# Kernel optimization log

Measured on AMD Instinct MI355X. Metric: run time of the kernel, lower is better.

The kernel has to match this reference:

```python
import jax, jax.numpy as jnp
import numpy as np

FM = 128       # feature_maps
QM = 128       # query_maps
ROUNDS = 4     # test_rounds (training=False)
N_VARS = 24576
N_CLAUSES = 98304
N_EDGES = 3 * N_CLAUSES
EPS = 1e-6


def _dense(k, fan_in, fan_out):
    return jax.random.normal(k, (fan_in, fan_out), jnp.float32) * (1.0 / np.sqrt(fan_in))


def setup_inputs() -> dict:
    key = jax.random.key(0)
    ks = jax.random.split(key, 20)
    return {
        "edge_lit": jax.random.randint(ks[0], (N_EDGES,), 0, 2 * N_VARS, dtype=jnp.int32),
        "edge_clause": jnp.sort(jax.random.randint(ks[1], (N_EDGES,), 0, N_CLAUSES, dtype=jnp.int32)),
        "noise_v": jax.random.normal(ks[2], (ROUNDS, N_VARS, 4), jnp.float32),
        "noise_c": jax.random.normal(ks[3], (ROUNDS, N_CLAUSES, 4), jnp.float32),
        # variables_query: MLP(2, QM, QM), input FM+4
        "vq_w0": _dense(ks[4], FM + 4, QM), "vq_b0": jnp.zeros((QM,), jnp.float32),
        "vq_w1": _dense(ks[5], QM, QM),     "vq_b1": jnp.zeros((QM,), jnp.float32),
        # clauses_query: MLP(2, QM, QM), input FM+4
        "cq_w0": _dense(ks[6], FM + 4, QM), "cq_b0": jnp.zeros((QM,), jnp.float32),
        "cq_w1": _dense(ks[7], QM, QM),     "cq_b1": jnp.zeros((QM,), jnp.float32),
        # clause_update: MLP(2, 2*FM, FM+QM), input FM+2*QM=384
        "cm_w0": _dense(ks[8], FM + 2 * QM, 2 * FM), "cm_b0": jnp.zeros((2 * FM,), jnp.float32),
        "cm_w1": _dense(ks[9], 2 * FM, FM + QM),     "cm_b1": jnp.zeros((FM + QM,), jnp.float32),
        # update_gate: MLP(3, 2*FM, FM), input QM+FM+2*QM=512
        "ug_w0": _dense(ks[10], QM + FM + 2 * QM, 2 * FM), "ug_b0": jnp.zeros((2 * FM,), jnp.float32),
        "ug_w1": _dense(ks[11], 2 * FM, 2 * FM),           "ug_b1": jnp.zeros((2 * FM,), jnp.float32),
        "ug_w2": _dense(ks[12], 2 * FM, FM),               "ug_b2": jnp.zeros((FM,), jnp.float32),
        # clauses_mask_output: MLP(2, FM, 1)
        "co_w0": _dense(ks[13], FM, FM), "co_b0": jnp.zeros((FM,), jnp.float32),
        "co_w1": _dense(ks[14], FM, 1),  "co_b1": jnp.zeros((1,), jnp.float32),
        "n_vars": N_VARS,
        "n_clauses": N_CLAUSES,
    }


def _forward(edge_lit, edge_clause, n_vars, n_clauses, floats):
    (noise_v, noise_c,
     vq_w0, vq_b0, vq_w1, vq_b1,
     cq_w0, cq_b0, cq_w1, cq_b1,
     cm_w0, cm_b0, cm_w1, cm_b1,
     ug_w0, ug_b0, ug_w1, ug_b1, ug_w2, ug_b2,
     co_w0, co_b0, co_w1, co_b1) = floats

    n_edges = edge_lit.shape[0]
    # lit_degree = row sums of sparse adjacency (all nonzeros are 1.0)
    lit_degree = jax.ops.segment_sum(jnp.ones((n_edges,), jnp.float32), edge_lit,
                                     num_segments=2 * n_vars)[:, None]          # [2V,1]
    degree_weight = jax.lax.rsqrt(jnp.maximum(lit_degree, 1.0))
    var_degree_weight = 4.0 * jax.lax.rsqrt(
        jnp.maximum(lit_degree[:n_vars] + lit_degree[n_vars:], 1.0))            # [V,1]

    def mlp2(x, w0, b0, w1, b1):
        return jax.nn.relu(x @ w0 + b0) @ w1 + b1

    def mlp3(x, w0, b0, w1, b1, w2, b2):
        h = jax.nn.relu(x @ w0 + b0)
        h = jax.nn.relu(h @ w1 + b1)
        return h @ w2 + b2

    def pair_norm(x):
        # PairNorm(subtract_mean=True), single graph -> global mean over nodes
        x = x - jnp.mean(x, axis=0, keepdims=True)
        return x * jax.lax.rsqrt(jnp.mean(jnp.square(x)) + EPS)

    def clauses_loss_fn(vq, cq):
        # unsat_cnf_clauses_loss: softplus literal values aggregated per clause,
        # clause satisfiability exp(-sum), gated by clause query mask.
        lits = jax.nn.softplus(jnp.concatenate([vq, -vq], axis=0))              # [2V,Q]
        csum = jax.ops.segment_sum(lits[edge_lit], edge_clause,
                                   num_segments=n_clauses)                      # [C,Q]
        loss = jnp.exp(-csum) * jax.nn.sigmoid(cq)
        return jnp.mean(loss), loss

    grad_fn = jax.grad(clauses_loss_fn, argnums=(0, 1), has_aux=True)

    def step(carry, xs):
        variables, clauses = carry
        nv, nc = xs
        vq = mlp2(jnp.concatenate([variables, nv], -1), vq_w0, vq_b0, vq_w1, vq_b1)
        cq = mlp2(jnp.concatenate([clauses, nc], -1), cq_w0, cq_b0, cq_w1, cq_b1)
        (vgrad, cgrad), clauses_loss = grad_fn(vq, cq)
        vgrad = vgrad * var_degree_weight
        clauses_loss = clauses_loss * 4.0
        clause_data = mlp2(jnp.concatenate([clauses, clauses_loss, cgrad], -1),
                           cm_w0, cm_b0, cm_w1, cm_b1)                          # [C,FM+QM]
        variables_loss_all = clause_data[:, :QM]
        clauses = pair_norm(clause_data[:, QM:]) * 0.25 + 0.1 * clauses
        # adj_matrix @ variables_loss_all (literal-side aggregation)
        variables_loss = jax.ops.segment_sum(variables_loss_all[edge_clause], edge_lit,
                                             num_segments=2 * n_vars) * degree_weight
        unit = jnp.concatenate([vgrad, variables,
                                variables_loss[:n_vars], variables_loss[n_vars:]], -1)
        variables = pair_norm(mlp3(unit, ug_w0, ug_b0, ug_w1, ug_b1, ug_w2, ug_b2)) * 0.25 \
                    + 0.1 * variables
        logits = mlp2(clauses, co_w0, co_b0, co_w1, co_b1)[:, 0]                # [C]
        return (variables, clauses), logits

    init = (jnp.ones((n_vars, FM), jnp.float32), jnp.ones((n_clauses, FM), jnp.float32))
    _, logits = jax.lax.scan(step, init, (noise_v, noise_c))                    # [R,C]
    return jax.nn.sigmoid(logits), jax.nn.softplus(logits)


def reference(edge_lit, edge_clause, noise_v, noise_c,
              vq_w0, vq_b0, vq_w1, vq_b1,
              cq_w0, cq_b0, cq_w1, cq_b1,
              cm_w0, cm_b0, cm_w1, cm_b1,
              ug_w0, ug_b0, ug_w1, ug_b1, ug_w2, ug_b2,
              co_w0, co_b0, co_w1, co_b1,
              n_vars, n_clauses):
    floats = (noise_v, noise_c,
              vq_w0, vq_b0, vq_w1, vq_b1,
              cq_w0, cq_b0, cq_w1, cq_b1,
              cm_w0, cm_b0, cm_w1, cm_b1,
              ug_w0, ug_b0, ug_w1, ug_b1, ug_w2, ug_b2,
              co_w0, co_b0, co_w1, co_b1)
    return _forward(edge_lit, edge_clause, int(n_vars), int(n_clauses), floats)
```

## Files before the change

### kernel.cpp

```cpp
#include <hip/hip_runtime.h>
#include <math.h>

#define NV 24576
#define NC 98304
#define NE 294912
#define CMCHUNK 24576

typedef unsigned short bf16;
typedef _Float16 f16;
using bf8 = __attribute__((ext_vector_type(8))) short;
using f4  = __attribute__((ext_vector_type(4))) float;

static constexpr float INV_CQM = 1.0f / 12582912.0f;
static constexpr float LOG2E = 1.44269504f;
static constexpr float LN2 = 0.69314718f;

__device__ __forceinline__ float b2f(bf16 h) { return __uint_as_float(((unsigned)h) << 16); }
__device__ __forceinline__ bf16 f2b(float f) {
  unsigned u = __float_as_uint(f);
  u += 0x7fff + ((u >> 16) & 1);
  return (bf16)(u >> 16);
}
__device__ __forceinline__ float fexp2(float x) { float r; asm("v_exp_f32 %0, %1" : "=v"(r) : "v"(x)); return r; }
__device__ __forceinline__ float flog2(float x) { float r; asm("v_log_f32 %0, %1" : "=v"(r) : "v"(x)); return r; }
__device__ __forceinline__ float frcpf(float x) { float r; asm("v_rcp_f32 %0, %1" : "=v"(r) : "v"(x)); return r; }
__device__ __forceinline__ float fsigm(float x) { return frcpf(1.0f + fexp2(-x * LOG2E)); }
__device__ __forceinline__ float fsoftplus(float x) {
  return fmaxf(x, 0.0f) + LN2 * flog2(1.0f + fexp2(-fabsf(x) * LOG2E));
}
__device__ __forceinline__ float cvt_ld(float x) { return x; }
__device__ __forceinline__ float cvt_ld(bf16 x) { return b2f(x); }

__device__ __forceinline__ void gload16(const void* g, void* l) {
  __builtin_amdgcn_global_load_lds((const __attribute__((address_space(1))) unsigned int*)g,
                                   (__attribute__((address_space(3))) unsigned int*)l, 16, 0, 0);
}


__global__ __launch_bounds__(256) void k_cptr(const int* __restrict__ ec, int* __restrict__ ptr) {
  int c = blockIdx.x * 256 + threadIdx.x;
  if (c > NC) return;
  int lo = 0, hi = NE;
  while (lo < hi) { int mid = (lo + hi) >> 1; if (ec[mid] < c) lo = mid + 1; else hi = mid; }
  ptr[c] = lo;
}

__global__ __launch_bounds__(256) void k_litcnt(const int* __restrict__ el, int* __restrict__ cnt) {
  int e = blockIdx.x * 256 + threadIdx.x;
  atomicAdd(&cnt[el[e]], 1);
}

__global__ __launch_bounds__(1024) void k_scan(int* __restrict__ cnt, int* __restrict__ ptr) {
  __shared__ int wsum[16];
  __shared__ int carry_s;
  int tid = threadIdx.x, lane = tid & 63, w = tid >> 6;
  if (tid == 0) carry_s = 0;
  __syncthreads();
  for (int base = 0; base < 2 * NV; base += 1024) {
    int x = cnt[base + tid];
    int v = x;
#pragma unroll
    for (int off = 1; off < 64; off <<= 1) {
      int y = __shfl_up(v, off, 64);
      if (lane >= off) v += y;
    }
    if (lane == 63) wsum[w] = v;
    __syncthreads();
    int carry = carry_s;
    int wpre = 0;
    for (int i = 0; i < w; ++i) wpre += wsum[i];
    int excl = carry + wpre + (v - x);
    ptr[base + tid] = excl;
    cnt[base + tid] = excl;
    __syncthreads();
    if (tid == 1023) carry_s = carry + wpre + v;
  }
  __syncthreads();
  if (tid == 0) ptr[2 * NV] = carry_s;
}

__global__ __launch_bounds__(256) void k_fillsort(const int* __restrict__ el, const int* __restrict__ ec,
                                                  int* __restrict__ cur, int* __restrict__ lclause) {
  int e = blockIdx.x * 256 + threadIdx.x;
  int pos = atomicAdd(&cur[el[e]], 1);
  lclause[pos] = ec[e];
}

__global__ __launch_bounds__(256) void k_degree(const int* __restrict__ lptr, float* __restrict__ dw,
                                                float* __restrict__ vdw) {
  int l = blockIdx.x * 256 + threadIdx.x;
  if (l < 2 * NV) dw[l] = rsqrtf(fmaxf((float)(lptr[l + 1] - lptr[l]), 1.0f));
  if (l < NV) {
    int d = (lptr[l + 1] - lptr[l]) + (lptr[l + NV + 1] - lptr[l + NV]);
    vdw[l] = 4.0f * rsqrtf(fmaxf((float)d, 1.0f));
  }
}

__global__ __launch_bounds__(256) void k_init_v(float* __restrict__ variables, bf16* __restrict__ ugA) {
  int i = blockIdx.x * 256 + threadIdx.x;
  variables[i] = 1.0f;
  ugA[(size_t)(i >> 7) * 512 + 128 + (i & 127)] = 0x3F80;
}
__global__ __launch_bounds__(256) void k_init_c(bf16* __restrict__ cmA) {
  int i = blockIdx.x * 256 + threadIdx.x;
  cmA[(size_t)(i >> 7) * 384 + (i & 127)] = 0x3F80;
}

__global__ __launch_bounds__(256) void k_wt(const float* __restrict__ w, bf16* __restrict__ wt,
                                            int K, int N, int Kpad) {
  int idx = blockIdx.x * 256 + threadIdx.x;
  int n = idx / Kpad, k = idx % Kpad;
  if (n >= N) return;
  wt[idx] = (k < K) ? f2b(w[(size_t)k * N + n]) : (bf16)0;
}


template <int KDIM, bool CONCAT, bool RELU, int OUT>
__global__ __launch_bounds__(256) void mgemm(const bf16* __restrict__ A0, int lda,
                                             const float* __restrict__ noise,
                                             const bf16* __restrict__ WT,
                                             const float* __restrict__ Bv,
                                             void* out0, void* out1, int ldOut) {
  __shared__ __align__(16) char smem[65536];
  constexpr int NT = KDIM / 64;
  const int tid = threadIdx.x;
  const int m0 = blockIdx.x * 128;
  const int n0 = blockIdx.y * 128;
  const int lane = tid & 63;
  const int w = tid >> 6;
  const int wr = w >> 1, wc = w & 1;
  const int rl = (tid >> 3) & 7;
  const int cc = tid & 7;
  const int swzoff = (cc * 16) ^ (rl << 4);

  auto stage = [&](int t, int buf) {
    char* As = smem + buf * 32768;
    char* Bs = As + 16384;
    const int k0 = t * 64;
    if (!CONCAT || k0 < 128) {
#pragma unroll
      for (int it = 0; it < 4; ++it) {
        int row0 = it * 32 + w * 8;
        int row = row0 + rl;
        gload16((const char*)(A0 + (size_t)(m0 + row) * lda + k0) + swzoff, As + row0 * 128);
        gload16((const char*)(WT + (size_t)(n0 + row) * KDIM + k0) + swzoff, Bs + row0 * 128);
      }
    } else {
      const int srow = tid >> 3, schunk = tid & 7;
#pragma unroll
      for (int it = 0; it < 4; ++it) {
        int row = srow + it * 32;
        alignas(16) bf16 tmp[8];
#pragma unroll
        for (int e = 0; e < 8; ++e) {
          int kk = schunk * 8 + e;
          tmp[e] = (kk < 4) ? f2b(noise[(size_t)(m0 + row) * 4 + kk]) : (bf16)0;
        }
        *reinterpret_cast<uint4*>(&As[row * 128 + ((schunk * 16) ^ ((row & 7) << 4))]) =
            *reinterpret_cast<uint4*>(tmp);
        int row0 = it * 32 + w * 8;
        gload16((const char*)(WT + (size_t)(n0 + row0 + rl) * KDIM + k0) + swzoff, Bs + row0 * 128);
      }
    }
  };

  f4 acc[4][4] = {};
  stage(0, 0);
#pragma unroll
  for (int t = 0; t < NT; ++t) {
    const int buf = t & 1;
    __builtin_amdgcn_sched_barrier(0);
    if (t + 1 < NT) {
      stage(t + 1, buf ^ 1);
      if (CONCAT && (t + 1) * 64 >= 128) {
        asm volatile("s_waitcnt vmcnt(4) lgkmcnt(0)" ::: "memory");
      } else {
        asm volatile("s_waitcnt vmcnt(8) lgkmcnt(0)" ::: "memory");
      }
    } else {
      asm volatile("s_waitcnt vmcnt(0) lgkmcnt(0)" ::: "memory");
    }
    __builtin_amdgcn_s_barrier();
    __builtin_amdgcn_sched_barrier(0);
    const char* As = smem + buf * 32768;
    const char* Bs = As + 16384;
#pragma unroll
    for (int kk = 0; kk < 2; ++kk) {
      bf8 a[4], b[4];
#pragma unroll
      for (int i = 0; i < 4; ++i) {
        int r = wr * 64 + i * 16 + (lane & 15);
        int cby = (kk * 64 + ((lane >> 4) * 16)) ^ ((r & 7) << 4);
        a[i] = *reinterpret_cast<const bf8*>(&As[r * 128 + cby]);
        int c = wc * 64 + i * 16 + (lane & 15);
        int cby2 = (kk * 64 + ((lane >> 4) * 16)) ^ ((c & 7) << 4);
        b[i] = *reinterpret_cast<const bf8*>(&Bs[c * 128 + cby2]);
      }
#pragma unroll
      for (int i = 0; i < 4; ++i)
#pragma unroll
        for (int j = 0; j < 4; ++j)
          acc[i][j] = __builtin_amdgcn_mfma_f32_16x16x32_bf16(a[i], b[j], acc[i][j], 0, 0, 0);
    }
    __builtin_amdgcn_sched_barrier(0);
    __builtin_amdgcn_s_barrier();
  }
  const int colloc = wc * 64 + (lane & 15);
  const int rowbase = m0 + wr * 64 + ((lane >> 4) << 2);
#pragma unroll
  for (int j = 0; j < 4; ++j) {
    int c = n0 + colloc + j * 16;
    float bias = Bv[c];
#pragma unroll
    for (int i = 0; i < 4; ++i) {
      int rb = rowbase + i * 16;
#pragma unroll
      for (int p = 0; p < 4; ++p) {
        float v = acc[i][j][p] + bias;
        if (RELU) v = fmaxf(v, 0.0f);
        int r = rb + p;
        if constexpr (OUT == 0) {
          ((float*)out0)[(size_t)r * ldOut + c] = v;
        } else if constexpr (OUT == 1) {
          ((bf16*)out0)[(size_t)r * ldOut + c] = f2b(v);
        } else if constexpr (OUT == 2) {
          bf16* o = (c < 128) ? (bf16*)out0 : (bf16*)out1;
          o[(size_t)r * 128 + (c & 127)] = f2b(v);
        } else {
          float tq = LN2 * flog2(1.0f + fexp2(-fabsf(v) * LOG2E));
          ((f16*)out0)[(size_t)r * 128 + c] = (f16)(fmaxf(v, 0.0f) + tq);
          ((f16*)out1)[(size_t)r * 128 + c] = (f16)(fmaxf(-v, 0.0f) + tq);
        }
      }
    }
  }
}


__global__ __launch_bounds__(256) void k_loss(const int* __restrict__ edge_lit, const int* __restrict__ cptr,
                                              const f16* __restrict__ spp, const f16* __restrict__ spn,
                                              const bf16* __restrict__ cq, bf16* __restrict__ cmA) {
  int c = blockIdx.x * 2 + (threadIdx.x >> 7);
  int q = threadIdx.x & 127;
  int e0 = cptr[c], e1 = cptr[c + 1];
  float csum = 0.0f;
  for (int e = e0; e < e1; ++e) {
    int lit = edge_lit[e];
    const f16* base = (lit < NV) ? (spp + (size_t)lit * 128) : (spn + (size_t)(lit - NV) * 128);
    csum += (float)base[q];
  }
  float s = fsigm(b2f(cq[(size_t)c * 128 + q]));
  float L = fexp2(-csum * LOG2E) * s;
  cmA[(size_t)c * 384 + 128 + q] = f2b(4.0f * L);
  cmA[(size_t)c * 384 + 256 + q] = f2b(L * (1.0f - s) * INV_CQM);
}

__global__ __launch_bounds__(256) void k_gatherv(const int* __restrict__ lptr, const int* __restrict__ lclause,
                                                 const bf16* __restrict__ cmA, const bf16* __restrict__ cd0,
                                                 const f16* __restrict__ spn, const float* __restrict__ dw,
                                                 const float* __restrict__ vdw, bf16* __restrict__ ugA) {
  int v = blockIdx.x;
  int half = threadIdx.x >> 7, q = threadIdx.x & 127;
  int l = v + half * NV;
  int j0 = lptr[l], j1 = lptr[l + 1];
  float sg = 0.0f, sv = 0.0f;
  for (int j = j0; j < j1; ++j) {
    int c = lclause[j];
    sg += b2f(cmA[(size_t)c * 384 + 128 + q]);
    sv += b2f(cd0[(size_t)c * 128 + q]);
  }
  __shared__ float sgl[2][128];
  sgl[half][q] = sg;
  ugA[(size_t)v * 512 + 256 + half * 128 + q] = f2b(sv * dw[l]);
  __syncthreads();
  if (half == 0) {
    float s = fexp2(-LOG2E * (float)spn[(size_t)v * 128 + q]);
    float g = ((1.0f - s) * sgl[1][q] - s * sgl[0][q]) * (INV_CQM * 0.25f) * vdw[v];
    ugA[(size_t)v * 512 + q] = f2b(g);
  }
}

template <typename T>
__global__ __launch_bounds__(256) void k_pn_stats(const T* __restrict__ X, int R, float* __restrict__ stats) {
  int q = threadIdx.x & 127;
  int rg = threadIdx.x >> 7;
  float cs = 0.0f, ss = 0.0f;
  for (int r = blockIdx.x * 2 + rg; r < R; r += gridDim.x * 2) {
    float x = cvt_ld(X[(size_t)r * 128 + q]);
    cs += x;
    ss += x * x;
  }
  __shared__ float scs[256], sss[256];
  scs[threadIdx.x] = cs;
  sss[threadIdx.x] = ss;
  __syncthreads();
  if (threadIdx.x < 128) atomicAdd(&stats[q], scs[q] + scs[128 + q]);
  for (int off = 128; off; off >>= 1) {
    if (threadIdx.x < off) sss[threadIdx.x] += sss[threadIdx.x + off];
    __syncthreads();
  }
  if (threadIdx.x == 0) atomicAdd(&stats[128], sss[0]);
}

__global__ __launch_bounds__(128) void k_pn_final(float* __restrict__ stats, float R) {
  __shared__ float s[128];
  int q = threadIdx.x;
  float m = stats[q] / R;
  s[q] = m * m;
  __syncthreads();
  for (int off = 64; off; off >>= 1) {
    if (q < off) s[q] += s[q + off];
    __syncthreads();
  }
  if (q == 0) {
    float var = (stats[128] - R * s[0]) / (R * 128.0f);
    stats[129] = rsqrtf(fmaxf(var, 0.0f) + 1e-6f) * 0.25f;
  }
  stats[q] = m;
}

__global__ __launch_bounds__(256) void k_pn_apply_c(const bf16* __restrict__ cd1, const float* __restrict__ stats,
                                                    bf16* __restrict__ cmA) {
  int i = blockIdx.x * 256 + threadIdx.x;
  int c = i >> 7, q = i & 127;
  float x = b2f(cd1[i]);
  float old = b2f(cmA[(size_t)c * 384 + q]);
  cmA[(size_t)c * 384 + q] = f2b((x - stats[q]) * stats[129] + 0.1f * old);
}

__global__ __launch_bounds__(256) void k_pn_apply_v(const float* __restrict__ uout, const float* __restrict__ stats,
                                                    float* __restrict__ variables, bf16* __restrict__ ugA) {
  int i = blockIdx.x * 256 + threadIdx.x;
  int v = i >> 7, q = i & 127;
  float nv = (uout[i] - stats[q]) * stats[129] + 0.1f * variables[i];
  variables[i] = nv;
  ugA[(size_t)v * 512 + 128 + q] = f2b(nv);
}

__global__ __launch_bounds__(256) void k_logits(const bf16* __restrict__ lh, const float* __restrict__ w1,
                                                const float* __restrict__ b1, float* __restrict__ outp, int t) {
  int wv = threadIdx.x >> 6, lane = threadIdx.x & 63;
  int c = blockIdx.x * 4 + wv;
  const bf16* row = lh + (size_t)c * 128;
  float v = b2f(row[lane]) * w1[lane] + b2f(row[64 + lane]) * w1[64 + lane];
#pragma unroll
  for (int off = 32; off; off >>= 1) v += __shfl_down(v, off, 64);
  if (lane == 0) {
    float lg = v + b1[0];
    outp[(size_t)t * NC + c] = fsigm(lg);
    outp[(size_t)4 * NC + (size_t)t * NC + c] = fsoftplus(lg);
  }
}


extern "C" void kernel_launch(void* const* d_in, const int* in_sizes, int n_in,
                              void* d_out, int out_size, void* d_ws, size_t ws_size,
                              hipStream_t stream) {
  const int* edge_lit = (const int*)d_in[0];
  const int* edge_clause = (const int*)d_in[1];
  const float* noise_v = (const float*)d_in[2];
  const float* noise_c = (const float*)d_in[3];
  const float* vq_w0 = (const float*)d_in[4];  const float* vq_b0 = (const float*)d_in[5];
  const float* vq_w1 = (const float*)d_in[6];  const float* vq_b1 = (const float*)d_in[7];
  const float* cq_w0 = (const float*)d_in[8];  const float* cq_b0 = (const float*)d_in[9];
  const float* cq_w1 = (const float*)d_in[10]; const float* cq_b1 = (const float*)d_in[11];
  const float* cm_w0 = (const float*)d_in[12]; const float* cm_b0 = (const float*)d_in[13];
  const float* cm_w1 = (const float*)d_in[14]; const float* cm_b1 = (const float*)d_in[15];
  const float* ug_w0 = (const float*)d_in[16]; const float* ug_b0 = (const float*)d_in[17];
  const float* ug_w1 = (const float*)d_in[18]; const float* ug_b1 = (const float*)d_in[19];
  const float* ug_w2 = (const float*)d_in[20]; const float* ug_b2 = (const float*)d_in[21];
  const float* co_w0 = (const float*)d_in[22]; const float* co_b0 = (const float*)d_in[23];
  const float* co_w1 = (const float*)d_in[24]; const float* co_b1 = (const float*)d_in[25];
  float* out = (float*)d_out;

  char* base = (char*)d_ws;
  size_t off = 0;
  auto A = [&](size_t n) -> char* {
    char* p = base + off;
    off = (off + n + 255) & ~(size_t)255;
    return p;
  };
  float* variables = (float*)A((size_t)NV * 128 * 4);
  bf16* cmA        = (bf16*)A((size_t)NC * 384 * 2);
  bf16* ugA        = (bf16*)A((size_t)NV * 512 * 2);
  char* R_cq       = A((size_t)NC * 128 * 2);
  char* R_h        = A((size_t)NC * 128 * 2);
  char* R_big      = A((size_t)2 * NV * 128 * 2 + (size_t)NV * 128 * 4);
  bf16* wtb        = (bf16*)A(983424);
  int* cptr = (int*)A((size_t)(NC + 1) * 4);
  int* lptr = (int*)A((size_t)(2 * NV + 1) * 4);
  int* lcur = (int*)A((size_t)2 * NV * 4);
  int* lclause = (int*)A((size_t)NE * 4);
  float* dw  = (float*)A((size_t)2 * NV * 4);
  float* vdw = (float*)A((size_t)NV * 4);
  float* stats = (float*)A(2048);
  if (off > ws_size) {
    hipMemsetAsync(d_out, 0xFF, (size_t)out_size * 4, stream);
    return;
  }

  bf16* cq  = (bf16*)R_cq;
  bf16* cd0 = (bf16*)R_cq;
  bf16* lh  = (bf16*)R_cq;
  bf16* hv  = (bf16*)R_h;
  bf16* hc  = (bf16*)R_h;
  bf16* cd1 = (bf16*)R_h;
  bf16* uh1 = (bf16*)R_h;
  bf16* uh2 = (bf16*)(R_h + (size_t)NV * 256 * 2);
  bf16* cmh = (bf16*)R_big;
  f16* spp  = (f16*)(R_big + 12582912);
  f16* spn  = spp + (size_t)NV * 128;
  float* uout = (float*)(R_big + 12582912);

  size_t wo = 0;
  auto WTa = [&](int n, int kp) { bf16* p = wtb + wo; wo += (size_t)n * kp; return p; };
  bf16* wt_vq0 = WTa(128, 192); bf16* wt_vq1 = WTa(128, 128);
  bf16* wt_cq0 = WTa(128, 192); bf16* wt_cq1 = WTa(128, 128);
  bf16* wt_cm0 = WTa(256, 384); bf16* wt_cm1 = WTa(256, 256);
  bf16* wt_ug0 = WTa(256, 512); bf16* wt_ug1 = WTa(256, 256);
  bf16* wt_ug2 = WTa(128, 256); bf16* wt_co0 = WTa(128, 128);

  hipMemsetAsync(lcur, 0, (size_t)2 * NV * 4, stream);
  k_cptr<<<(NC + 256) / 256, 256, 0, stream>>>(edge_clause, cptr);
  k_litcnt<<<NE / 256, 256, 0, stream>>>(edge_lit, lcur);
  k_scan<<<1, 1024, 0, stream>>>(lcur, lptr);
  k_fillsort<<<NE / 256, 256, 0, stream>>>(edge_lit, edge_clause, lcur, lclause);
  k_degree<<<(2 * NV + 255) / 256, 256, 0, stream>>>(lptr, dw, vdw);
  k_init_v<<<NV * 128 / 256, 256, 0, stream>>>(variables, ugA);
  k_init_c<<<NC * 128 / 256, 256, 0, stream>>>(cmA);
  k_wt<<<128 * 192 / 256, 256, 0, stream>>>(vq_w0, wt_vq0, 132, 128, 192);
  k_wt<<<128 * 128 / 256, 256, 0, stream>>>(vq_w1, wt_vq1, 128, 128, 128);
  k_wt<<<128 * 192 / 256, 256, 0, stream>>>(cq_w0, wt_cq0, 132, 128, 192);
  k_wt<<<128 * 128 / 256, 256, 0, stream>>>(cq_w1, wt_cq1, 128, 128, 128);
  k_wt<<<256 * 384 / 256, 256, 0, stream>>>(cm_w0, wt_cm0, 384, 256, 384);
  k_wt<<<256 * 256 / 256, 256, 0, stream>>>(cm_w1, wt_cm1, 256, 256, 256);
  k_wt<<<256 * 512 / 256, 256, 0, stream>>>(ug_w0, wt_ug0, 512, 256, 512);
  k_wt<<<256 * 256 / 256, 256, 0, stream>>>(ug_w1, wt_ug1, 256, 256, 256);
  k_wt<<<128 * 256 / 256, 256, 0, stream>>>(ug_w2, wt_ug2, 256, 128, 256);
  k_wt<<<128 * 128 / 256, 256, 0, stream>>>(co_w0, wt_co0, 128, 128, 128);

  for (int t = 0; t < 4; ++t) {
    const float* nvp = noise_v + (size_t)t * NV * 4;
    const float* ncp = noise_c + (size_t)t * NC * 4;
    mgemm<192, true, true, 1><<<dim3(NV / 128, 1), 256, 0, stream>>>(ugA + 128, 512, nvp, wt_vq0, vq_b0, hv, nullptr, 128);
    mgemm<128, false, false, 3><<<dim3(NV / 128, 1), 256, 0, stream>>>(hv, 128, nullptr, wt_vq1, vq_b1, spp, spn, 128);
    mgemm<192, true, true, 1><<<dim3(NC / 128, 1), 256, 0, stream>>>(cmA, 384, ncp, wt_cq0, cq_b0, hc, nullptr, 128);
    mgemm<128, false, false, 1><<<dim3(NC / 128, 1), 256, 0, stream>>>(hc, 128, nullptr, wt_cq1, cq_b1, cq, nullptr, 128);
    k_loss<<<NC / 2, 256, 0, stream>>>(edge_lit, cptr, spp, spn, cq, cmA);
    for (int ch = 0; ch < NC / CMCHUNK; ++ch) {
      size_t ro = (size_t)ch * CMCHUNK;
      mgemm<384, false, true, 1><<<dim3(CMCHUNK / 128, 2), 256, 0, stream>>>(cmA + ro * 384, 384, nullptr, wt_cm0, cm_b0, cmh, nullptr, 256);
      mgemm<256, false, false, 2><<<dim3(CMCHUNK / 128, 2), 256, 0, stream>>>(cmh, 256, nullptr, wt_cm1, cm_b1, cd0 + ro * 128, cd1 + ro * 128, 128);
    }
    k_gatherv<<<NV, 256, 0, stream>>>(lptr, lclause, cmA, cd0, spn, dw, vdw, ugA);
    hipMemsetAsync(stats, 0, 132 * 4, stream);
    k_pn_stats<bf16><<<256, 256, 0, stream>>>(cd1, NC, stats);
    k_pn_final<<<1, 128, 0, stream>>>(stats, (float)NC);
    k_pn_apply_c<<<NC * 128 / 256, 256, 0, stream>>>(cd1, stats, cmA);
    mgemm<128, false, true, 1><<<dim3(NC / 128, 1), 256, 0, stream>>>(cmA, 384, nullptr, wt_co0, co_b0, lh, nullptr, 128);
    k_logits<<<NC / 4, 256, 0, stream>>>(lh, co_w1, co_b1, out, t);
    mgemm<512, false, true, 1><<<dim3(NV / 128, 2), 256, 0, stream>>>(ugA, 512, nullptr, wt_ug0, ug_b0, uh1, nullptr, 256);
    mgemm<256, false, true, 1><<<dim3(NV / 128, 2), 256, 0, stream>>>(uh1, 256, nullptr, wt_ug1, ug_b1, uh2, nullptr, 256);
    mgemm<256, false, false, 0><<<dim3(NV / 128, 1), 256, 0, stream>>>(uh2, 256, nullptr, wt_ug2, ug_b2, uout, nullptr, 128);
    hipMemsetAsync(stats, 0, 132 * 4, stream);
    k_pn_stats<float><<<256, 256, 0, stream>>>(uout, NV, stats);
    k_pn_final<<<1, 128, 0, stream>>>(stats, (float)NV);
    k_pn_apply_v<<<NV * 128 / 256, 256, 0, stream>>>(uout, stats, variables, ugA);
  }
}
```

Baseline: 1.988 ms.

## Fuse logits head into output GEMM and batch gather loops

Adds a GEMM epilogue mode that applies the ReLU, the 128-to-1 projection, bias, sigmoid and softplus in place. This removes the intermediate lh buffer and the separate k_logits launch. k_loss now handles 8 clauses per thread group, indexes spp/spn as one array, and unrolls edge loads by four. k_gatherv gets the same four-way unrolled gather to expose more memory-level parallelism. The fused epilogue adds shuffles and a shared-memory reduction, and it assumes spn sits directly after spp.

```diff
diff --git a/kernel.cpp b/kernel.cpp
--- a/kernel.cpp
+++ b/kernel.cpp
@@ -207,6 +207,52 @@
   }
   const int colloc = wc * 64 + (lane & 15);
   const int rowbase = m0 + wr * 64 + ((lane >> 4) << 2);
+
+  if constexpr (OUT == 4) {
+    const float* w1 = (const float*)out1;
+    float* outp = (float*)out0;
+    const int t = ldOut;
+    float part[4][4];
+#pragma unroll
+    for (int i = 0; i < 4; ++i)
+#pragma unroll
+      for (int p = 0; p < 4; ++p) part[i][p] = 0.0f;
+#pragma unroll
+    for (int j = 0; j < 4; ++j) {
+      int c = colloc + j * 16;
+      float bias = Bv[c];
+      float w1c = w1[c];
+#pragma unroll
+      for (int i = 0; i < 4; ++i)
+#pragma unroll
+        for (int p = 0; p < 4; ++p)
+          part[i][p] += fmaxf(acc[i][j][p] + bias, 0.0f) * w1c;
+    }
+#pragma unroll
+    for (int m = 1; m < 16; m <<= 1)
+#pragma unroll
+      for (int i = 0; i < 4; ++i)
+#pragma unroll
+        for (int p = 0; p < 4; ++p)
+          part[i][p] += __shfl_xor(part[i][p], m, 64);
+    float* red = (float*)smem;
+    if ((lane & 15) == 0) {
+#pragma unroll
+      for (int i = 0; i < 4; ++i)
+#pragma unroll
+        for (int p = 0; p < 4; ++p)
+          red[wc * 128 + wr * 64 + i * 16 + ((lane >> 4) << 2) + p] = part[i][p];
+    }
+    __syncthreads();
+    if (tid < 128) {
+      float lg = red[tid] + red[128 + tid] + noise[0];
+      int row = m0 + tid;
+      outp[(size_t)t * NC + row] = fsigm(lg);
+      outp[(size_t)4 * NC + (size_t)t * NC + row] = fsoftplus(lg);
+    }
+    return;
+  }
+
 #pragma unroll
   for (int j = 0; j < 4; ++j) {
     int c = n0 + colloc + j * 16;
@@ -238,21 +284,31 @@
 
 
 __global__ __launch_bounds__(256) void k_loss(const int* __restrict__ edge_lit, const int* __restrict__ cptr,
-                                              const f16* __restrict__ spp, const f16* __restrict__ spn,
-                                              const bf16* __restrict__ cq, bf16* __restrict__ cmA) {
-  int c = blockIdx.x * 2 + (threadIdx.x >> 7);
-  int q = threadIdx.x & 127;
-  int e0 = cptr[c], e1 = cptr[c + 1];
-  float csum = 0.0f;
-  for (int e = e0; e < e1; ++e) {
-    int lit = edge_lit[e];
-    const f16* base = (lit < NV) ? (spp + (size_t)lit * 128) : (spn + (size_t)(lit - NV) * 128);
-    csum += (float)base[q];
-  }
-  float s = fsigm(b2f(cq[(size_t)c * 128 + q]));
-  float L = fexp2(-csum * LOG2E) * s;
-  cmA[(size_t)c * 384 + 128 + q] = f2b(4.0f * L);
-  cmA[(size_t)c * 384 + 256 + q] = f2b(L * (1.0f - s) * INV_CQM);
+                                              const f16* __restrict__ sp, const bf16* __restrict__ cq,
+                                              bf16* __restrict__ cmA) {
+  const int g = threadIdx.x >> 7;
+  const int q = threadIdx.x & 127;
+  const int c0 = blockIdx.x * 16 + g * 8;
+#pragma unroll
+  for (int ci = 0; ci < 8; ++ci) {
+    int c = c0 + ci;
+    int e0 = cptr[c], e1 = cptr[c + 1];
+    float csum = 0.0f;
+    for (int e = e0; e < e1; e += 4) {
+#pragma unroll
+      for (int k = 0; k < 4; ++k) {
+        int ee = e + k;
+        bool ok = ee < e1;
+        int lit = ok ? edge_lit[ee] : 0;
+        float v = ok ? (float)sp[(size_t)lit * 128 + q] : 0.0f;
+        csum += v;
+      }
+    }
+    float s = fsigm(b2f(cq[(size_t)c * 128 + q]));
+    float L = fexp2(-csum * LOG2E) * s;
+    cmA[(size_t)c * 384 + 128 + q] = f2b(4.0f * L);
+    cmA[(size_t)c * 384 + 256 + q] = f2b(L * (1.0f - s) * INV_CQM);
+  }
 }
 
 __global__ __launch_bounds__(256) void k_gatherv(const int* __restrict__ lptr, const int* __restrict__ lclause,
@@ -264,10 +320,17 @@
   int l = v + half * NV;
   int j0 = lptr[l], j1 = lptr[l + 1];
   float sg = 0.0f, sv = 0.0f;
-  for (int j = j0; j < j1; ++j) {
-    int c = lclause[j];
-    sg += b2f(cmA[(size_t)c * 384 + 128 + q]);
-    sv += b2f(cd0[(size_t)c * 128 + q]);
+  for (int j = j0; j < j1; j += 4) {
+#pragma unroll
+    for (int k = 0; k < 4; ++k) {
+      int jj = j + k;
+      bool ok = jj < j1;
+      int c = ok ? lclause[jj] : 0;
+      float a = ok ? b2f(cmA[(size_t)c * 384 + 128 + q]) : 0.0f;
+      float b = ok ? b2f(cd0[(size_t)c * 128 + q]) : 0.0f;
+      sg += a;
+      sv += b;
+    }
   }
   __shared__ float sgl[2][128];
   sgl[half][q] = sg;
@@ -335,21 +398,6 @@
   float nv = (uout[i] - stats[q]) * stats[129] + 0.1f * variables[i];
   variables[i] = nv;
   ugA[(size_t)v * 512 + 128 + q] = f2b(nv);
-}
-
-__global__ __launch_bounds__(256) void k_logits(const bf16* __restrict__ lh, const float* __restrict__ w1,
-                                                const float* __restrict__ b1, float* __restrict__ outp, int t) {
-  int wv = threadIdx.x >> 6, lane = threadIdx.x & 63;
-  int c = blockIdx.x * 4 + wv;
-  const bf16* row = lh + (size_t)c * 128;
-  float v = b2f(row[lane]) * w1[lane] + b2f(row[64 + lane]) * w1[64 + lane];
-#pragma unroll
-  for (int off = 32; off; off >>= 1) v += __shfl_down(v, off, 64);
-  if (lane == 0) {
-    float lg = v + b1[0];
-    outp[(size_t)t * NC + c] = fsigm(lg);
-    outp[(size_t)4 * NC + (size_t)t * NC + c] = fsoftplus(lg);
-  }
 }
 
 
@@ -401,7 +449,6 @@
 
   bf16* cq  = (bf16*)R_cq;
   bf16* cd0 = (bf16*)R_cq;
-  bf16* lh  = (bf16*)R_cq;
   bf16* hv  = (bf16*)R_h;
   bf16* hc  = (bf16*)R_h;
   bf16* cd1 = (bf16*)R_h;
@@ -446,7 +493,7 @@
     mgemm<128, false, false, 3><<<dim3(NV / 128, 1), 256, 0, stream>>>(hv, 128, nullptr, wt_vq1, vq_b1, spp, spn, 128);
     mgemm<192, true, true, 1><<<dim3(NC / 128, 1), 256, 0, stream>>>(cmA, 384, ncp, wt_cq0, cq_b0, hc, nullptr, 128);
     mgemm<128, false, false, 1><<<dim3(NC / 128, 1), 256, 0, stream>>>(hc, 128, nullptr, wt_cq1, cq_b1, cq, nullptr, 128);
-    k_loss<<<NC / 2, 256, 0, stream>>>(edge_lit, cptr, spp, spn, cq, cmA);
+    k_loss<<<NC / 16, 256, 0, stream>>>(edge_lit, cptr, spp, cq, cmA);
     for (int ch = 0; ch < NC / CMCHUNK; ++ch) {
       size_t ro = (size_t)ch * CMCHUNK;
       mgemm<384, false, true, 1><<<dim3(CMCHUNK / 128, 2), 256, 0, stream>>>(cmA + ro * 384, 384, nullptr, wt_cm0, cm_b0, cmh, nullptr, 256);
@@ -457,8 +504,7 @@
     k_pn_stats<bf16><<<256, 256, 0, stream>>>(cd1, NC, stats);
     k_pn_final<<<1, 128, 0, stream>>>(stats, (float)NC);
     k_pn_apply_c<<<NC * 128 / 256, 256, 0, stream>>>(cd1, stats, cmA);
-    mgemm<128, false, true, 1><<<dim3(NC / 128, 1), 256, 0, stream>>>(cmA, 384, nullptr, wt_co0, co_b0, lh, nullptr, 128);
-    k_logits<<<NC / 4, 256, 0, stream>>>(lh, co_w1, co_b1, out, t);
+    mgemm<128, false, false, 4><<<dim3(NC / 128, 1), 256, 0, stream>>>(cmA, 384, co_b1, wt_co0, co_b0, out, (void*)co_w1, t);
     mgemm<512, false, true, 1><<<dim3(NV / 128, 2), 256, 0, stream>>>(ugA, 512, nullptr, wt_ug0, ug_b0, uh1, nullptr, 256);
     mgemm<256, false, true, 1><<<dim3(NV / 128, 2), 256, 0, stream>>>(uh1, 256, nullptr, wt_ug1, ug_b1, uh2, nullptr, 256);
     mgemm<256, false, false, 0><<<dim3(NV / 128, 1), 256, 0, stream>>>(uh2, 256, nullptr, wt_ug2, ug_b2, uout, nullptr, 128);
```

Measured after the change: 1.940 ms. 1.02x faster.
